# Performance work log

Hardware: AMD Instinct MI355X
Metric: run time of the kernel (lower is better)

The kernel has to match this reference:

```python
import jax, jax.numpy as jnp
import numpy as np

B, L, S, H, E, D = 4, 2048, 2048, 8, 64, 64

def setup_inputs() -> dict:
    key = jax.random.key(0)
    kq, kk, kv = jax.random.split(key, 3)
    queries = jax.random.normal(kq, (B, L, H, E), dtype=jnp.float32)
    keys = jax.random.normal(kk, (B, S, H, E), dtype=jnp.float32)
    values = jax.random.normal(kv, (B, S, H, D), dtype=jnp.float32)
    # TriangularCausalMask: True above the diagonal (positions to mask)
    causal = jnp.triu(jnp.ones((L, S), dtype=bool), k=1)
    attn_mask = jnp.broadcast_to(causal[None, None], (B, 1, L, S))
    return {"queries": queries, "keys": keys, "values": values, "attn_mask": attn_mask}

def reference(queries, keys, values, attn_mask):
    scale = 1.0 / jnp.sqrt(jnp.asarray(E, queries.dtype))
    # scores: [B,H,L,S]
    scores = jnp.einsum('blhe,bshe->bhls', queries, keys)
    neg_inf = jnp.asarray(-jnp.inf, scores.dtype)
    scores = jnp.where(attn_mask, neg_inf, scores)
    A = jax.nn.softmax(scale * scores, axis=-1)
    # dropout is identity in eval mode
    V = jnp.einsum('bhls,bshd->blhd', A, values)
    return V
```

## Files before the change

### kernel.cpp

```cpp
#include <hip/hip_runtime.h>
#include <math.h>

typedef __attribute__((ext_vector_type(8))) short bf16x8;
typedef __attribute__((ext_vector_type(4))) float f32x4;
typedef __attribute__((ext_vector_type(4))) unsigned int u32x4;

#define B_ 4
#define L_ 2048
#define S_ 2048
#define H_ 8
#define E_ 64
#define D_ 64
#define NT_ 32
#define TILE_BYTES 16384
#define WS_NEEDED ((size_t)B_ * H_ * NT_ * TILE_BYTES)
#define SCL (0.125f * 1.44269504088896f)

__device__ __forceinline__ unsigned short f2bf(float x) {
    unsigned int u = __builtin_bit_cast(unsigned int, x);
    u += 0x7fffu + ((u >> 16) & 1u);
    return (unsigned short)(u >> 16);
}
__device__ __forceinline__ int rho(int r) {
    return (r & 32) | (((r >> 2) & 1) << 4) | (((r >> 3) & 3) << 2) | (r & 3);
}
__device__ __forceinline__ void gload16(const void* g, void* l) {
    __builtin_amdgcn_global_load_lds((const __attribute__((address_space(1))) unsigned int*)g,
                                     (__attribute__((address_space(3))) unsigned int*)l, 16, 0, 0);
}

__global__ __launch_bounds__(256) void prep_kv(const float* __restrict__ K,
                                               const float* __restrict__ V,
                                               unsigned short* __restrict__ ws)
{
    __shared__ __align__(16) unsigned short vt[64][80];
    const int tid = threadIdx.x;
    const int bid = blockIdx.x;
    const int kt  = bid >> 5;
    const int bh  = (((bid >> 3) & 3) << 3) | (bid & 7);
    const int b   = bh >> 3, h = bh & 7;
    const int s0  = kt * 64;
    const int r   = tid >> 2;
    const int e0  = (tid & 3) * 16;

    const float* krow = K + (((size_t)(b * S_ + s0 + r)) * H_ + h) * E_ + e0;
    const float* vrow = V + (((size_t)(b * S_ + s0 + r)) * H_ + h) * D_ + e0;
    char* tile = (char*)(ws) + ((size_t)(bh * NT_ + kt) * TILE_BYTES);

    unsigned short kb[16];
    #pragma unroll
    for (int i = 0; i < 4; ++i) {
        f32x4 k4 = *(const f32x4*)(krow + i * 4);
        #pragma unroll
        for (int jq = 0; jq < 4; ++jq) kb[i * 4 + jq] = f2bf(k4[jq]);
    }
    {
        const int rr = rho(r);
        const int m  = (rr & 7) << 4;
        char* kbase = tile + rr * 128;
        u32x4 lo, hi;
        #pragma unroll
        for (int jq = 0; jq < 4; ++jq) {
            lo[jq] = (unsigned)kb[2 * jq] | ((unsigned)kb[2 * jq + 1] << 16);
            hi[jq] = (unsigned)kb[8 + 2 * jq] | ((unsigned)kb[9 + 2 * jq] << 16);
        }
        *(u32x4*)(kbase + ((2 * e0) ^ m))      = lo;
        *(u32x4*)(kbase + ((2 * e0 + 16) ^ m)) = hi;
    }
    #pragma unroll
    for (int i = 0; i < 4; ++i) {
        f32x4 v4 = *(const f32x4*)(vrow + i * 4);
        #pragma unroll
        for (int jq = 0; jq < 4; ++jq) vt[e0 + i * 4 + jq][r] = f2bf(v4[jq]);
    }
    __syncthreads();
    {
        const int d  = tid >> 2;
        const int c0 = (tid & 3) * 16;
        const int m  = (d & 7) << 4;
        char* vbase = tile + 8192 + d * 128;
        u32x4 lo = *(const u32x4*)&vt[d][c0];
        u32x4 hi = *(const u32x4*)&vt[d][c0 + 8];
        *(u32x4*)(vbase + ((2 * c0) ^ m))      = lo;
        *(u32x4*)(vbase + ((2 * c0 + 16) ^ m)) = hi;
    }
}

__global__ __launch_bounds__(256, 2) void attn17(const float* __restrict__ Q,
                                                 const unsigned short* __restrict__ ws,
                                                 float* __restrict__ O)
{
    __shared__ __align__(16) char pool[4 * 16384];

    const int tid  = threadIdx.x;
    const int lane = tid & 63;
    const int w    = tid >> 6;
    const int lq   = lane & 15;
    const int gl   = lane >> 4;

    const int bid = blockIdx.x;
    const int bh  = bid & 31;
    const int q   = bid >> 5;
    const int jj  = (q < 8) ? (15 - q) : (q - 8);
    const int b0  = bh >> 3, h = bh & 7;

    const int nt = 2 * jj + 2;
    const int c  = 2 * jj + (w >> 1);
    const int q0 = jj * 128 + w * 32;
    int qrow[2];
    qrow[0] = q0 + lq;
    qrow[1] = q0 + 16 + lq;

    bf16x8 qf[2][2];
    #pragma unroll
    for (int qs = 0; qs < 2; ++qs) {
        const float* qptr = Q + (((size_t)(b0 * L_ + qrow[qs])) * H_ + h) * E_;
        #pragma unroll
        for (int eb = 0; eb < 2; ++eb) {
            const float* pq = qptr + eb * 32 + gl * 8;
            f32x4 a = *(const f32x4*)pq;
            f32x4 b = *(const f32x4*)(pq + 4);
            bf16x8 qv;
            #pragma unroll
            for (int k = 0; k < 4; ++k) {
                qv[k]     = (short)f2bf(a[k] * SCL);
                qv[4 + k] = (short)f2bf(b[k] * SCL);
            }
            qf[qs][eb] = qv;
        }
    }

    f32x4 acc[2][4] = {};
    float ls[2] = {0.f, 0.f};

    const char* tb = (const char*)ws + (size_t)bh * NT_ * TILE_BYTES;

    #define STAGE17(T, BUF) do { \
        const char* gp_ = tb + (size_t)(T) * TILE_BYTES + tid * 16; \
        char* lp_ = pool + (BUF) * 16384 + tid * 16; \
        gload16(gp_, lp_);                 gload16(gp_ + 4096, lp_ + 4096); \
        gload16(gp_ + 8192, lp_ + 8192);   gload16(gp_ + 12288, lp_ + 12288); \
    } while (0)

    STAGE17(0, 0);
    STAGE17(1, 1);
    for (int i = 0; i < nt; ++i) {
        if (i + 2 < nt) STAGE17(i + 2, (i + 2) & 3);
        const int rem = nt - 1 - i;
        if (rem >= 2)      asm volatile("s_waitcnt vmcnt(8)" ::: "memory");
        else if (rem == 1) asm volatile("s_waitcnt vmcnt(4)" ::: "memory");
        else               asm volatile("s_waitcnt vmcnt(0)" ::: "memory");
        __builtin_amdgcn_s_barrier();
        __builtin_amdgcn_sched_barrier(0);

        if (i <= c) {
            const char* Kl = pool + (i & 3) * 16384;
            const char* Vl = Kl + 8192;
            const int kv0 = i * 64;
            const bool maskit = (i == c);

            u32x4 pw[2][2];
            #pragma unroll
            for (int st = 0; st < 4; ++st) {
                const int row = st * 16 + lq;
                const int mm = (row & 7) << 4;
                const char* kr = Kl + row * 128;
                bf16x8 k0 = *(const bf16x8*)(kr + ((16 * gl) ^ mm));
                bf16x8 k1 = *(const bf16x8*)(kr + ((64 + 16 * gl) ^ mm));
                #pragma unroll
                for (int qs = 0; qs < 2; ++qs) {
                    f32x4 z = {0.f, 0.f, 0.f, 0.f};
                    __builtin_amdgcn_s_setprio(1);
                    f32x4 cc = __builtin_amdgcn_mfma_f32_16x16x32_bf16(k0, qf[qs][0], z, 0, 0, 0);
                    cc = __builtin_amdgcn_mfma_f32_16x16x32_bf16(k1, qf[qs][1], cc, 0, 0, 0);
                    __builtin_amdgcn_s_setprio(0);
                    if (maskit) {
                        #pragma unroll
                        for (int r = 0; r < 4; ++r) {
                            const int kv = kv0 + 32 * (st >> 1) + 8 * gl + 4 * (st & 1) + r;
                            if (kv > qrow[qs]) cc[r] = -INFINITY;
                        }
                    }
                    f32x4 ev;
                    #pragma unroll
                    for (int r = 0; r < 4; ++r)
                        asm("v_exp_f32 %0, %1" : "=v"(ev[r]) : "v"(cc[r]));
                    ls[qs] += (ev[0] + ev[1]) + (ev[2] + ev[3]);
                    asm("v_cvt_pk_bf16_f32 %0, %1, %2" : "=v"(pw[qs][st >> 1][2 * (st & 1)])     : "v"(ev[0]), "v"(ev[1]));
                    asm("v_cvt_pk_bf16_f32 %0, %1, %2" : "=v"(pw[qs][st >> 1][2 * (st & 1) + 1]) : "v"(ev[2]), "v"(ev[3]));
                }
            }

            #pragma unroll
            for (int dt = 0; dt < 4; ++dt) {
                const int row = dt * 16 + lq;
                const int mm = (row & 7) << 4;
                bf16x8 v0 = *(const bf16x8*)(Vl + row * 128 + ((16 * gl) ^ mm));
                bf16x8 v1 = *(const bf16x8*)(Vl + row * 128 + ((64 + 16 * gl) ^ mm));
                __builtin_amdgcn_s_setprio(1);
                #pragma unroll
                for (int qs = 0; qs < 2; ++qs) {
                    acc[qs][dt] = __builtin_amdgcn_mfma_f32_16x16x32_bf16(v0, __builtin_bit_cast(bf16x8, pw[qs][0]), acc[qs][dt], 0, 0, 0);
                    acc[qs][dt] = __builtin_amdgcn_mfma_f32_16x16x32_bf16(v1, __builtin_bit_cast(bf16x8, pw[qs][1]), acc[qs][dt], 0, 0, 0);
                }
                __builtin_amdgcn_s_setprio(0);
            }
        }
    }
    #undef STAGE17

    #pragma unroll
    for (int qs = 0; qs < 2; ++qs) {
        float l = ls[qs] + __shfl_xor(ls[qs], 16);
        l += __shfl_xor(l, 32);
        const float inv = 1.0f / l;
        float* op = O + (((size_t)(b0 * L_ + qrow[qs])) * H_ + h) * D_;
        #pragma unroll
        for (int dt = 0; dt < 4; ++dt) {
            f32x4 o;
            #pragma unroll
            for (int r = 0; r < 4; ++r) o[r] = acc[qs][dt][r] * inv;
            *(f32x4*)(op + dt * 16 + 4 * gl) = o;
        }
    }
}

#define KPITCH 72
__global__ __launch_bounds__(256, 2) void attn_fwd_fb(
    const float* __restrict__ Q, const float* __restrict__ K,
    const float* __restrict__ V, float* __restrict__ O)
{
    __shared__ unsigned short Klds[64 * KPITCH];
    __shared__ unsigned short Vlds[64 * KPITCH];
    const int tid = threadIdx.x, lane = tid & 63, w = tid >> 6;
    const int lq = lane & 15, g = lane >> 4;
    const int bid = blockIdx.x, qb = bid & 31, bh = bid >> 5;
    const int b0 = bh >> 3, h = bh & 7;
    const int q0 = qb * 64, qrow = q0 + w * 16 + lq;
    const float* qptr = Q + ((size_t)(b0 * L_ + qrow) * H_ + h) * E_;
    bf16x8 qf[2];
    #pragma unroll
    for (int eb = 0; eb < 2; ++eb) {
        const float* pp = qptr + eb * 32 + g * 8;
        f32x4 a = *(const f32x4*)pp; f32x4 b = *(const f32x4*)(pp + 4);
        bf16x8 qv;
        #pragma unroll
        for (int jq = 0; jq < 4; ++jq) { qv[jq] = (short)f2bf(a[jq] * 0.125f); qv[4 + jq] = (short)f2bf(b[jq] * 0.125f); }
        qf[eb] = qv;
    }
    const int tr = tid >> 2, tc = tid & 3;
    const int rh = rho(tr);
    f32x4 acc[4] = {};
    float mrow = -INFINITY, lrow = 0.f;
    for (int kt = 0; kt < qb + 1; ++kt) {
        const int kv0 = kt * 64;
        __syncthreads();
        {
            const float* krow = K + ((size_t)((b0 * S_ + kv0 + tr)) * H_ + h) * E_;
            const float* vrow = V + ((size_t)((b0 * S_ + kv0 + tr)) * H_ + h) * D_;
            #pragma unroll
            for (int i = 0; i < 4; ++i) {
                const int e0 = tc * 4 + i * 16;
                f32x4 k4 = *(const f32x4*)(krow + e0);
                unsigned int lo = (unsigned)f2bf(k4[0]) | ((unsigned)f2bf(k4[1]) << 16);
                unsigned int hi = (unsigned)f2bf(k4[2]) | ((unsigned)f2bf(k4[3]) << 16);
                *(uint2*)&Klds[rh * KPITCH + e0] = make_uint2(lo, hi);
                f32x4 v4 = *(const f32x4*)(vrow + e0);
                #pragma unroll
                for (int k2 = 0; k2 < 4; ++k2) Vlds[(e0 + k2) * KPITCH + tr] = f2bf(v4[k2]);
            }
        }
        __syncthreads();
        f32x4 sc[4];
        #pragma unroll
        for (int st = 0; st < 4; ++st) {
            const unsigned short* kr = &Klds[(st * 16 + lq) * KPITCH];
            bf16x8 ka0 = *(const bf16x8*)(kr + 8 * g);
            bf16x8 ka1 = *(const bf16x8*)(kr + 32 + 8 * g);
            f32x4 cc = {0.f, 0.f, 0.f, 0.f};
            cc = __builtin_amdgcn_mfma_f32_16x16x32_bf16(ka0, qf[0], cc, 0, 0, 0);
            cc = __builtin_amdgcn_mfma_f32_16x16x32_bf16(ka1, qf[1], cc, 0, 0, 0);
            sc[st] = cc;
        }
        float tmax = -INFINITY;
        #pragma unroll
        for (int st = 0; st < 4; ++st) {
            const int kvb = kv0 + 32 * (st >> 1) + 8 * g + 4 * (st & 1);
            #pragma unroll
            for (int r = 0; r < 4; ++r) { if (kvb + r > qrow) sc[st][r] = -INFINITY; tmax = fmaxf(tmax, sc[st][r]); }
        }
        tmax = fmaxf(tmax, __shfl_xor(tmax, 16));
        tmax = fmaxf(tmax, __shfl_xor(tmax, 32));
        const float mnew = fmaxf(mrow, tmax);
        const float corr = __expf(mrow - mnew);
        float pv[4][4]; float tsum = 0.f;
        #pragma unroll
        for (int st = 0; st < 4; ++st)
            #pragma unroll
            for (int r = 0; r < 4; ++r) { float e = __expf(sc[st][r] - mnew); pv[st][r] = e; tsum += e; }
        tsum += __shfl_xor(tsum, 16); tsum += __shfl_xor(tsum, 32);
        lrow = lrow * corr + tsum; mrow = mnew;
        #pragma unroll
        for (int dt = 0; dt < 4; ++dt)
            #pragma unroll
            for (int r = 0; r < 4; ++r) acc[dt][r] *= corr;
        bf16x8 pb[2];
        #pragma unroll
        for (int bb = 0; bb < 2; ++bb)
            #pragma unroll
            for (int s = 0; s < 2; ++s)
                #pragma unroll
                for (int r = 0; r < 4; ++r) pb[bb][4 * s + r] = (short)f2bf(pv[2 * bb + s][r]);
        #pragma unroll
        for (int bb = 0; bb < 2; ++bb)
            #pragma unroll
            for (int dt = 0; dt < 4; ++dt) {
                bf16x8 va = *(const bf16x8*)&Vlds[(dt * 16 + lq) * KPITCH + 32 * bb + 8 * g];
                acc[dt] = __builtin_amdgcn_mfma_f32_16x16x32_bf16(va, pb[bb], acc[dt], 0, 0, 0);
            }
    }
    const float inv = 1.0f / lrow;
    float* optr = O + ((size_t)(b0 * L_ + qrow) * H_ + h) * D_;
    #pragma unroll
    for (int dt = 0; dt < 4; ++dt) {
        f32x4 o;
        #pragma unroll
        for (int r = 0; r < 4; ++r) o[r] = acc[dt][r] * inv;
        *(f32x4*)(optr + dt * 16 + 4 * g) = o;
    }
}

extern "C" void kernel_launch(void* const* d_in, const int* in_sizes, int n_in,
                              void* d_out, int out_size, void* d_ws, size_t ws_size,
                              hipStream_t stream) {
    const float* Q = (const float*)d_in[0];
    const float* K = (const float*)d_in[1];
    const float* V = (const float*)d_in[2];
    float* O = (float*)d_out;
    if (ws_size >= WS_NEEDED) {
        prep_kv<<<dim3(B_ * H_ * NT_), 256, 0, stream>>>(K, V, (unsigned short*)d_ws);
        attn17<<<dim3(512), 256, 0, stream>>>(Q, (const unsigned short*)d_ws, O);
    } else {
        attn_fwd_fb<<<dim3(B_ * H_ * 32), 256, 0, stream>>>(Q, K, V, O);
    }
}
```

Baseline: 46.95 us.

## Split long causal KV ranges into chunks with partial-sum combine kernel

Each long query block's KV loop is split into chunks of up to eight tiles, giving 1280 blocks in place of 512. Partial numerators are written to O (chunk 0) or to bf16 workspace buffers (other chunks), and row sums go to per-chunk arrays. A new combine kernel adds the partials and normalizes. The LDS ring drops from four to two buffers and occupancy is raised to four blocks per CU, with an extra barrier per tile. The costs are an extra kernel launch, extra global traffic, and bf16 rounding of the partial accumulators. The workspace requirement also grows, so smaller workspaces fall back to the slow path.

```diff
diff --git a/kernel.cpp b/kernel.cpp
--- a/kernel.cpp
+++ b/kernel.cpp
@@ -2,6 +2,7 @@
 #include <math.h>
 
 typedef __attribute__((ext_vector_type(8))) short bf16x8;
+typedef __attribute__((ext_vector_type(8))) unsigned short u16x8;
 typedef __attribute__((ext_vector_type(4))) float f32x4;
 typedef __attribute__((ext_vector_type(4))) unsigned int u32x4;
 
@@ -13,7 +14,12 @@
 #define D_ 64
 #define NT_ 32
 #define TILE_BYTES 16384
-#define WS_NEEDED ((size_t)B_ * H_ * NT_ * TILE_BYTES)
+#define IMG_BYTES ((size_t)B_ * H_ * NT_ * TILE_BYTES)
+#define PSZ ((size_t)B_ * L_ * H_ * D_ * 2)
+#define PK_OFF(k) (IMG_BYTES + (size_t)((k) - 1) * PSZ)
+#define LARR_OFF(c) (IMG_BYTES + 3 * PSZ + (size_t)(c) * (B_ * H_ * L_ * 4))
+#define WS_NEEDED  IMG_BYTES
+#define WS2_NEEDED (IMG_BYTES + 3 * PSZ + 4 * (size_t)(B_ * H_ * L_ * 4))
 #define SCL (0.125f * 1.44269504088896f)
 
 __device__ __forceinline__ unsigned short f2bf(float x) {
@@ -86,11 +92,19 @@
     }
 }
 
-__global__ __launch_bounds__(256, 2) void attn17(const float* __restrict__ Q,
+__device__ __constant__ const signed char JJ_TAB[40] = {
+    15,15,15,15, 14,14,14, 13,13,13, 12,12,12, 11,11,11, 10,10, 9,9, 8,8, 7,7, 6, 5, 4, 3,
+    14,10,6,2,  13,9,5,1,  12,8,4,0 };
+__device__ __constant__ const signed char CC_TAB[40] = {
+    0,1,2,3, 0,1,2, 0,1,2, 0,1,2, 0,1,2, 0,1, 0,1, 0,1, 0,1, 0, 0, 0, 0,
+    3,2,1,0, 3,2,1,0, 3,2,1,0 };
+
+__global__ __launch_bounds__(256, 4) void attn19(const float* __restrict__ Q,
                                                  const unsigned short* __restrict__ ws,
-                                                 float* __restrict__ O)
+                                                 float* __restrict__ O,
+                                                 char* __restrict__ wsc)
 {
-    __shared__ __align__(16) char pool[4 * 16384];
+    __shared__ __align__(16) char pool[2 * 16384];
 
     const int tid  = threadIdx.x;
     const int lane = tid & 63;
@@ -100,13 +114,17 @@
 
     const int bid = blockIdx.x;
     const int bh  = bid & 31;
-    const int q   = bid >> 5;
-    const int jj  = (q < 8) ? (15 - q) : (q - 8);
+    const int idx = bid >> 5;
+    const int jj  = JJ_TAB[idx];
+    const int cch = CC_TAB[idx];
     const int b0  = bh >> 3, h = bh & 7;
 
-    const int nt = 2 * jj + 2;
-    const int c  = 2 * jj + (w >> 1);
-    const int q0 = jj * 128 + w * 32;
+    const int nt  = 2 * jj + 2;
+    const int nch = (jj >> 2) + 1;
+    const int kb  = cch * 8;
+    int ke = kb + 8; if (ke > nt) ke = nt;
+    const int cw  = 2 * jj + (w >> 1);
+    const int q0  = jj * 128 + w * 32;
     int qrow[2];
     qrow[0] = q0 + lq;
     qrow[1] = q0 + 16 + lq;
@@ -135,29 +153,30 @@
 
     const char* tb = (const char*)ws + (size_t)bh * NT_ * TILE_BYTES;
 
-    #define STAGE17(T, BUF) do { \
+    #define STAGE19(T, BUF) do { \
         const char* gp_ = tb + (size_t)(T) * TILE_BYTES + tid * 16; \
         char* lp_ = pool + (BUF) * 16384 + tid * 16; \
         gload16(gp_, lp_);                 gload16(gp_ + 4096, lp_ + 4096); \
         gload16(gp_ + 8192, lp_ + 8192);   gload16(gp_ + 12288, lp_ + 12288); \
     } while (0)
 
-    STAGE17(0, 0);
-    STAGE17(1, 1);
-    for (int i = 0; i < nt; ++i) {
-        if (i + 2 < nt) STAGE17(i + 2, (i + 2) & 3);
-        const int rem = nt - 1 - i;
-        if (rem >= 2)      asm volatile("s_waitcnt vmcnt(8)" ::: "memory");
-        else if (rem == 1) asm volatile("s_waitcnt vmcnt(4)" ::: "memory");
-        else               asm volatile("s_waitcnt vmcnt(0)" ::: "memory");
+    STAGE19(kb, 0);
+    int cur = 0;
+    for (int kt = kb; kt < ke; ++kt) {
+        if (kt + 1 < ke) {
+            STAGE19(kt + 1, cur ^ 1);
+            asm volatile("s_waitcnt vmcnt(4)" ::: "memory");
+        } else {
+            asm volatile("s_waitcnt vmcnt(0)" ::: "memory");
+        }
         __builtin_amdgcn_s_barrier();
         __builtin_amdgcn_sched_barrier(0);
 
-        if (i <= c) {
-            const char* Kl = pool + (i & 3) * 16384;
+        if (kt <= cw) {
+            const char* Kl = pool + cur * 16384;
             const char* Vl = Kl + 8192;
-            const int kv0 = i * 64;
-            const bool maskit = (i == c);
+            const int kv0 = kt * 64;
+            const bool maskit = (kt == cw);
 
             u32x4 pw[2][2];
             #pragma unroll
@@ -206,23 +225,80 @@
                 __builtin_amdgcn_s_setprio(0);
             }
         }
-    }
-    #undef STAGE17
+        __builtin_amdgcn_s_barrier();
+        cur ^= 1;
+    }
+    #undef STAGE19
 
     #pragma unroll
     for (int qs = 0; qs < 2; ++qs) {
         float l = ls[qs] + __shfl_xor(ls[qs], 16);
         l += __shfl_xor(l, 32);
-        const float inv = 1.0f / l;
-        float* op = O + (((size_t)(b0 * L_ + qrow[qs])) * H_ + h) * D_;
-        #pragma unroll
-        for (int dt = 0; dt < 4; ++dt) {
-            f32x4 o;
-            #pragma unroll
-            for (int r = 0; r < 4; ++r) o[r] = acc[qs][dt][r] * inv;
-            *(f32x4*)(op + dt * 16 + 4 * gl) = o;
-        }
-    }
+        const size_t obase = (((size_t)(b0 * L_ + qrow[qs])) * H_ + h) * D_;
+        if (nch == 1) {
+            const float inv = 1.0f / l;
+            float* op = O + obase;
+            #pragma unroll
+            for (int dt = 0; dt < 4; ++dt) {
+                f32x4 o;
+                #pragma unroll
+                for (int r = 0; r < 4; ++r) o[r] = acc[qs][dt][r] * inv;
+                *(f32x4*)(op + dt * 16 + 4 * gl) = o;
+            }
+        } else {
+            float* lc = (float*)(wsc + LARR_OFF(cch));
+            if (lane < 16) lc[(b0 * H_ + h) * L_ + qrow[qs]] = l;
+            if (cch == 0) {
+                float* op = O + obase;
+                #pragma unroll
+                for (int dt = 0; dt < 4; ++dt)
+                    *(f32x4*)(op + dt * 16 + 4 * gl) = acc[qs][dt];
+            } else {
+                unsigned short* pp = (unsigned short*)(wsc + PK_OFF(cch)) + obase;
+                #pragma unroll
+                for (int dt = 0; dt < 4; ++dt) {
+                    unsigned int w0, w1;
+                    asm("v_cvt_pk_bf16_f32 %0, %1, %2" : "=v"(w0) : "v"(acc[qs][dt][0]), "v"(acc[qs][dt][1]));
+                    asm("v_cvt_pk_bf16_f32 %0, %1, %2" : "=v"(w1) : "v"(acc[qs][dt][2]), "v"(acc[qs][dt][3]));
+                    *(uint2*)(pp + dt * 16 + 4 * gl) = make_uint2(w0, w1);
+                }
+            }
+        }
+    }
+}
+
+__global__ __launch_bounds__(256) void combine19(float* __restrict__ O,
+                                                 const char* __restrict__ wsc)
+{
+    const int f = (blockIdx.x * 256 + threadIdx.x) * 8;
+    const int l = (f >> 9) & (L_ - 1);
+    const int jj = l >> 7;
+    if (jj < 4) return;
+    const int nch = (jj >> 2) + 1;
+    const int h = (f >> 6) & 7;
+    const int b = f >> 20;
+    const int li = (b * 8 + h) * L_ + l;
+
+    float lt = ((const float*)(wsc + LARR_OFF(0)))[li]
+             + ((const float*)(wsc + LARR_OFF(1)))[li];
+    f32x4 a0 = *(f32x4*)(O + f);
+    f32x4 a1 = *(f32x4*)(O + f + 4);
+    #pragma unroll
+    for (int k = 1; k <= 3; ++k) {
+        if (k >= nch) break;
+        u16x8 pb = *(const u16x8*)((const unsigned short*)(wsc + PK_OFF(k)) + f);
+        #pragma unroll
+        for (int r = 0; r < 4; ++r) {
+            a0[r] += __builtin_bit_cast(float, (unsigned)pb[r] << 16);
+            a1[r] += __builtin_bit_cast(float, (unsigned)pb[4 + r] << 16);
+        }
+        if (k >= 2) lt += ((const float*)(wsc + LARR_OFF(k)))[li];
+    }
+    const float inv = 1.0f / lt;
+    #pragma unroll
+    for (int r = 0; r < 4; ++r) { a0[r] *= inv; a1[r] *= inv; }
+    *(f32x4*)(O + f)     = a0;
+    *(f32x4*)(O + f + 4) = a1;
 }
 
 #define KPITCH 72
@@ -337,9 +413,10 @@
     const float* K = (const float*)d_in[1];
     const float* V = (const float*)d_in[2];
     float* O = (float*)d_out;
-    if (ws_size >= WS_NEEDED) {
+    if (ws_size >= WS2_NEEDED) {
         prep_kv<<<dim3(B_ * H_ * NT_), 256, 0, stream>>>(K, V, (unsigned short*)d_ws);
-        attn17<<<dim3(512), 256, 0, stream>>>(Q, (const unsigned short*)d_ws, O);
+        attn19<<<dim3(1280), 256, 0, stream>>>(Q, (const unsigned short*)d_ws, O, (char*)d_ws);
+        combine19<<<dim3(2048), 256, 0, stream>>>(O, (const char*)d_ws);
     } else {
         attn_fwd_fb<<<dim3(B_ * H_ * 32), 256, 0, stream>>>(Q, K, V, O);
     }
```

Result: slower. 48.91 us (+4.2%).
